# Kernel tuning notes

Hardware: AMD Instinct MI355X
Metric: run time of the kernel (lower is better)

## Reference

```python
import jax, jax.numpy as jnp
import numpy as np

B, N, D, H, L = 4, 1024, 256, 4, 2  # batch, nodes, mem_dim, heads, gcn sublayers
DK = D // H


def setup_inputs() -> dict:
    key = jax.random.key(0)
    ks = jax.random.split(key, 12)
    s = 0.05  # weight scale
    return {
        "gcn_inputs": jax.random.normal(ks[0], (B, N, D), jnp.float32),
        "rel_embs": jax.random.normal(ks[1], (B, N, D), jnp.float32),
        "adj": jax.random.randint(ks[2], (B, N, N), 0, 2, jnp.int32),
        "mask": jnp.zeros((B, 1, N), jnp.int32),  # 0 == valid token in this code's convention
        "W_Q": jax.random.normal(ks[3], (2 * D, D), jnp.float32) * s,
        "b_Q": jnp.zeros((D,), jnp.float32),
        "W_K": jax.random.normal(ks[4], (D, D), jnp.float32) * s,
        "b_K": jnp.zeros((D,), jnp.float32),
        "W_gcn": jax.random.normal(ks[5], (H * L, D, D), jnp.float32) * s,
        "b_gcn": jnp.zeros((H * L, D), jnp.float32),
        "W_out": jax.random.normal(ks[6], (D * H * L, D), jnp.float32) * s,
        "b_out": jnp.zeros((D,), jnp.float32),
    }


def _zscore_attn(scores, m, adj):
    """Faithful port of stdzscore + threshold + weightsoftmax chain.
    scores: [B,H,N,N]; m: bool [B,1,1,N] True=valid; adj: int [B,N,N]."""
    mf = m.astype(scores.dtype)
    # mymean (dim=[-1]): count from mask squeezed over dim -2 -> [B,1], +1e-4
    cnt_mean = mf[:, :, 0, :].sum(-1)[..., None] + 1e-4  # [B,1,1]
    ds = jnp.where(m, scores, 0.0).sum(-1)               # [B,H,N]
    mean = ds / cnt_mean                                  # [B,H,N]
    # mystd (dim=[-1]): count from full mask summed over -1 -> [B,1,1], +1e-4
    cnt_std = mf.sum(-1) + 1e-4                           # [B,1,1]
    sdata = jnp.where(m, (scores - mean[..., None]) ** 2, 0.0).sum(-1)
    std = jnp.sqrt(sdata / cnt_std + 1e-10)               # [B,H,N]
    z = (scores - mean[..., None]) / (std[..., None] + 1e-4)
    z = jnp.where(m, z, 0.0)
    thresh = z < 0
    s2 = jnp.where(thresh, -1e9, z)
    s2 = jnp.where(m, s2, -1e9)
    # weightsoftmax: stable exp, multiply by adjacency, mask, renormalize
    e = jnp.exp(s2 - s2.max(-1, keepdims=True))
    e = e * adj.astype(scores.dtype)[:, None]             # [B,H,N,N]
    e = jnp.where(m, e, 0.0) + 1e-10
    w = e / e.sum(-1, keepdims=True)
    w = jnp.where(m, w, 0.0)
    kill = (~m) | thresh | (adj == 0)[:, None]
    return jnp.where(kill, 0.0, w)


def reference(gcn_inputs, rel_embs, adj, mask, W_Q, b_Q, W_K, b_K, W_gcn, b_gcn, W_out, b_out):
    m = (mask == 0)[:, :, None, :]  # [B,1,1,N] True = valid
    # MultiHeadAttention: q from cat(query, rel), k from query
    q = (jnp.concatenate([gcn_inputs, rel_embs], -1) @ W_Q + b_Q)
    q = q.reshape(B, N, H, DK).transpose(0, 2, 1, 3)      # [B,H,N,DK]
    k = (gcn_inputs @ W_K + b_K).reshape(B, N, H, DK).transpose(0, 2, 1, 3)
    scores = jnp.einsum('bhnd,bhmd->bhnm', q, k)
    p_attn = _zscore_attn(scores, m, adj)                 # [B,H,N,N]
    # MultiGraphConvLayer (dropout = identity at inference)
    head_outs = []
    for i in range(H):
        a = p_attn[:, i]                                  # [B,N,N]
        denom = a.sum(2, keepdims=True) + 1.0             # [B,N,1]
        outputs = gcn_inputs
        layer_outs = []
        for l in range(L):
            idx = i * L + l
            Ax = jnp.einsum('bnm,bmd->bnd', a, outputs)
            # Linear applied to BOTH Ax and outputs (bias added twice, as in source)
            AxW = (Ax @ W_gcn[idx] + b_gcn[idx]) + (outputs @ W_gcn[idx] + b_gcn[idx])
            outputs = jax.nn.relu(AxW / denom)
            layer_outs.append(outputs)
        head_outs.append(jnp.concatenate(layer_outs, -1))  # [B,N,D*L]
    final = jnp.concatenate(head_outs, -1)                 # [B,N,D*L*H]
    return gcn_inputs + final @ W_out + b_out
```

## Files before the change

### kernel.cpp

```cpp
#include <hip/hip_runtime.h>
#include <math.h>

typedef unsigned short u16;
typedef __attribute__((ext_vector_type(8))) short short8;
typedef __attribute__((ext_vector_type(4))) float floatx4;

#define LDS_P 72

__device__ __forceinline__ float bf2f(u16 u) {
  union { unsigned int i; float f; } v; v.i = ((unsigned int)u) << 16; return v.f;
}
__device__ __forceinline__ u16 f2bf(float f) {
  union { float f; unsigned int i; } v; v.f = f;
  unsigned int x = v.i;
  return (u16)((x + 0x7FFFu + ((x >> 16) & 1u)) >> 16);
}

__device__ __forceinline__ void stage64(const u16* __restrict__ G, int ldg,
                                        u16* __restrict__ S, int tid) {
#pragma unroll
  for (int j = 0; j < 2; ++j) {
    int id = tid + (j << 8);
    int row = id >> 3, c8 = (id & 7) << 3;
    *reinterpret_cast<float4*>(S + row * LDS_P + c8) =
        *reinterpret_cast<const float4*>(G + (long long)row * ldg + c8);
  }
}

__device__ __forceinline__ void mfma_loop(const u16* __restrict__ A, int lda,
                                          const u16* __restrict__ Bt, int ldb,
                                          int K, u16* As, u16* Bs,
                                          floatx4 acc[2][2], int tid) {
  int lane = tid & 63;
  int wm = ((tid >> 6) & 1) << 5, wn = ((tid >> 6) >> 1) << 5;
  int lr = lane & 15, lq8 = (lane >> 4) << 3;
  for (int k0 = 0; k0 < K; k0 += 64) {
    stage64(A + k0, lda, As, tid);
    stage64(Bt + k0, ldb, Bs, tid);
    __syncthreads();
#pragma unroll
    for (int kc = 0; kc < 64; kc += 32) {
      short8 a0 = *reinterpret_cast<const short8*>(As + (wm + lr) * LDS_P + kc + lq8);
      short8 a1 = *reinterpret_cast<const short8*>(As + (wm + 16 + lr) * LDS_P + kc + lq8);
      short8 b0 = *reinterpret_cast<const short8*>(Bs + (wn + lr) * LDS_P + kc + lq8);
      short8 b1 = *reinterpret_cast<const short8*>(Bs + (wn + 16 + lr) * LDS_P + kc + lq8);
      acc[0][0] = __builtin_amdgcn_mfma_f32_16x16x32_bf16(a0, b0, acc[0][0], 0, 0, 0);
      acc[0][1] = __builtin_amdgcn_mfma_f32_16x16x32_bf16(a0, b1, acc[0][1], 0, 0, 0);
      acc[1][0] = __builtin_amdgcn_mfma_f32_16x16x32_bf16(a1, b0, acc[1][0], 0, 0, 0);
      acc[1][1] = __builtin_amdgcn_mfma_f32_16x16x32_bf16(a1, b1, acc[1][1], 0, 0, 0);
    }
    __syncthreads();
  }
}

#define EPI_SETUP                                                     \
  int lane = threadIdx.x & 63;                                        \
  int wm = ((threadIdx.x >> 6) & 1) << 5,                             \
      wn = ((threadIdx.x >> 6) >> 1) << 5;                            \
  int lr = lane & 15, lq4 = (lane >> 4) << 2;

__global__ __launch_bounds__(256) void proj2_k(
    const u16* __restrict__ A, const u16* __restrict__ WQT,
    const u16* __restrict__ WKT, const float* __restrict__ b_Q,
    const float* __restrict__ b_K, u16* __restrict__ qbf,
    u16* __restrict__ kbf) {
  __shared__ u16 As[64 * LDS_P], Bs[64 * LDS_P];
  int z = blockIdx.z;
  int m0 = blockIdx.y << 6, n0 = blockIdx.x << 6;
  int K = z ? 256 : 512, ldb = z ? 256 : 512;
  const u16* Bt = z ? WKT : WQT;
  const float* bias = z ? b_K : b_Q;
  u16* C = z ? kbf : qbf;
  floatx4 acc[2][2] = {};
  mfma_loop(A + (long long)m0 * 512, 512, Bt + (long long)n0 * ldb, ldb, K, As, Bs,
            acc, threadIdx.x);
  EPI_SETUP
#pragma unroll
  for (int ti = 0; ti < 2; ++ti)
#pragma unroll
    for (int tj = 0; tj < 2; ++tj)
#pragma unroll
      for (int r = 0; r < 4; ++r) {
        int row = m0 + wm + ti * 16 + lq4 + r;
        int col = n0 + wn + tj * 16 + lr;
        C[(long long)row * 256 + col] = f2bf(acc[ti][tj][r] + bias[col]);
      }
}

__global__ __launch_bounds__(256) void mscore_k(
    const u16* __restrict__ q, const u16* __restrict__ kb,
    u16* __restrict__ sc) {
  __shared__ u16 As[64 * LDS_P], Bs[64 * LDS_P];
  int z = blockIdx.z;
  int b = z & 3, h = z >> 2;
  int m0 = blockIdx.y << 6, n0 = blockIdx.x << 6;
  const u16* Ab = q + b * 262144 + h * 64;
  const u16* Bb = kb + b * 262144 + h * 64;
  floatx4 acc[2][2] = {};
  mfma_loop(Ab + (long long)m0 * 256, 256, Bb + (long long)n0 * 256, 256, 64, As, Bs,
            acc, threadIdx.x);
  u16* Cb = sc + ((long long)z << 20);
  EPI_SETUP
#pragma unroll
  for (int ti = 0; ti < 2; ++ti)
#pragma unroll
    for (int tj = 0; tj < 2; ++tj)
#pragma unroll
      for (int r = 0; r < 4; ++r) {
        int row = m0 + wm + ti * 16 + lq4 + r;
        int col = n0 + wn + tj * 16 + lr;
        Cb[(long long)row * 1024 + col] = f2bf(acc[ti][tj][r]);
      }
}

__device__ __forceinline__ float wred_sum(float v) {
#pragma unroll
  for (int m = 32; m > 0; m >>= 1) v += __shfl_xor(v, m, 64);
  return v;
}
__device__ __forceinline__ void wred_sum2(float& a, float& b) {
#pragma unroll
  for (int m = 32; m > 0; m >>= 1) {
    float ta = __shfl_xor(a, m, 64);
    float tb = __shfl_xor(b, m, 64);
    a += ta; b += tb;
  }
}
__device__ __forceinline__ float wred_max(float v) {
#pragma unroll
  for (int m = 32; m > 0; m >>= 1) v = fmaxf(v, __shfl_xor(v, m, 64));
  return v;
}

__global__ __launch_bounds__(256) void zscore_w(
    const u16* __restrict__ sc, const int* __restrict__ adj,
    const int* __restrict__ mask, u16* __restrict__ wout,
    float* __restrict__ denh) {
  int wv = threadIdx.x >> 6, lane = threadIdx.x & 63;
  int row = (blockIdx.x << 2) + wv;
  int b = row >> 10, n = row & 1023;
  int e0 = lane << 4;
  const int* arow = adj + ((long long)row << 10) + e0;
  const int* mrow = mask + (b << 10) + e0;

  unsigned int vbits = 0, abits = 0;
#pragma unroll
  for (int q = 0; q < 4; ++q) {
    int4 a4 = *reinterpret_cast<const int4*>(arow + (q << 2));
    int4 m4 = *reinterpret_cast<const int4*>(mrow + (q << 2));
    vbits |= (unsigned)(m4.x == 0) << (q * 4);
    vbits |= (unsigned)(m4.y == 0) << (q * 4 + 1);
    vbits |= (unsigned)(m4.z == 0) << (q * 4 + 2);
    vbits |= (unsigned)(m4.w == 0) << (q * 4 + 3);
    abits |= (unsigned)(a4.x != 0) << (q * 4);
    abits |= (unsigned)(a4.y != 0) << (q * 4 + 1);
    abits |= (unsigned)(a4.z != 0) << (q * 4 + 2);
    abits |= (unsigned)(a4.w != 0) << (q * 4 + 3);
  }
  float cnt = wred_sum((float)__popc(vbits));
  float cnteff = cnt + 0.0001f;

  for (int h = 0; h < 4; ++h) {
    int z = (h << 2) + b;
    const u16* srow = sc + ((long long)z << 20) + ((long long)n << 10) + e0;
    float s[16];
#pragma unroll
    for (int q = 0; q < 2; ++q) {
      uint4 u = *reinterpret_cast<const uint4*>(srow + (q << 3));
      unsigned int uu[4] = {u.x, u.y, u.z, u.w};
#pragma unroll
      for (int t = 0; t < 4; ++t) {
        union { unsigned int i; float f; } lo, hi;
        lo.i = uu[t] << 16;
        hi.i = uu[t] & 0xffff0000u;
        s[q * 8 + t * 2] = lo.f;
        s[q * 8 + t * 2 + 1] = hi.f;
      }
    }
    float suml = 0.f, sql = 0.f;
#pragma unroll
    for (int u = 0; u < 16; ++u)
      if ((vbits >> u) & 1) { suml += s[u]; sql += s[u] * s[u]; }
    wred_sum2(suml, sql);
    float mean = suml / cnteff;
    float sdata = sql - 2.f * mean * suml + cnt * mean * mean;
    float stdv = sqrtf(fmaxf(sdata, 0.f) / cnteff + 1e-10f);
    float inv = 1.f / (stdv + 0.0001f);

    float maxl = -1e9f;
#pragma unroll
    for (int u = 0; u < 16; ++u) {
      float zz = (s[u] - mean) * inv;
      int vv = (vbits >> u) & 1;
      zz = vv ? zz : 0.f;
      s[u] = zz;
      if (vv && zz >= 0.f) maxl = fmaxf(maxl, zz);
    }
    float rowmax = wred_max(maxl);

    float e[16], el = 0.f;
#pragma unroll
    for (int u = 0; u < 16; ++u) {
      int vv = (vbits >> u) & 1, aa = (abits >> u) & 1;
      float ev = (vv && aa && (s[u] >= 0.f)) ? expf(s[u] - rowmax) : 0.f;
      e[u] = ev + 1e-10f;
      el += e[u];
    }
    float esum = wred_sum(el);
    float rinv = 1.f / esum;

    float wl = 0.f;
    unsigned int wo[8];
#pragma unroll
    for (int u = 0; u < 16; u += 2) {
      int s0 = ((vbits >> u) & 1) && ((abits >> u) & 1) && (s[u] >= 0.f);
      int s1 = ((vbits >> (u + 1)) & 1) && ((abits >> (u + 1)) & 1) && (s[u + 1] >= 0.f);
      float w0 = s0 ? e[u] * rinv : 0.f;
      float w1 = s1 ? e[u + 1] * rinv : 0.f;
      wl += w0 + w1;
      wo[u >> 1] = (unsigned)f2bf(w0) | ((unsigned)f2bf(w1) << 16);
    }
    float wsum = wred_sum(wl);

    u16* orow = wout + ((size_t)z << 20) + ((size_t)n << 10) + e0;
    reinterpret_cast<uint4*>(orow)[0] = make_uint4(wo[0], wo[1], wo[2], wo[3]);
    reinterpret_cast<uint4*>(orow)[1] = make_uint4(wo[4], wo[5], wo[6], wo[7]);
    if (lane == 0) denh[(z << 10) + n] = wsum + 1.0f;
  }
}

__global__ __launch_bounds__(256) void gcn_k(
    const u16* __restrict__ wght, const u16* __restrict__ srcT,
    const u16* __restrict__ addsrc, int zmask, int ldadd, long long sAdd,
    const u16* __restrict__ WgT_all, const float* __restrict__ bg_all,
    const float* __restrict__ den, int l,
    u16* __restrict__ ob, u16* __restrict__ obT, u16* __restrict__ fin) {
  __shared__ u16 lds[35328];
  u16* As = lds;
  u16* Bs = lds + 4608;
  u16* Ts = lds;
  u16* Ws = lds + 16896;
  int tid = threadIdx.x;
  int m0 = blockIdx.x << 6;
  int z = blockIdx.y;
  int lane = tid & 63, w = tid >> 6;
  int lr = lane & 15, lq8 = (lane >> 4) << 3, lq4 = (lane >> 4) << 2;

  const u16* Aw = wght + ((long long)z << 20) + (long long)m0 * 1024;
  const u16* Bt = srcT + (long long)(z & zmask) * 262144;
  const u16* addb = addsrc + (long long)(z & zmask) * sAdd;
  int idx2 = (z >> 2) * 2 + l;
  const u16* Wg = WgT_all + (long long)idx2 * 65536;

  floatx4 acc[4][4] = {};
  for (int k0 = 0; k0 < 1024; k0 += 64) {
#pragma unroll
    for (int j = 0; j < 2; ++j) {
      int id = tid + (j << 8);
      int row = id >> 3, c8 = (id & 7) << 3;
      *reinterpret_cast<float4*>(As + row * 72 + c8) =
          *reinterpret_cast<const float4*>(Aw + (long long)row * 1024 + k0 + c8);
    }
#pragma unroll
    for (int j = 0; j < 8; ++j) {
      int id = tid + (j << 8);
      int row = id >> 3, c8 = (id & 7) << 3;
      *reinterpret_cast<float4*>(Bs + row * 72 + c8) =
          *reinterpret_cast<const float4*>(Bt + (long long)row * 1024 + k0 + c8);
    }
    __syncthreads();
#pragma unroll
    for (int kc = 0; kc < 64; kc += 32) {
      short8 a[4], b[4];
#pragma unroll
      for (int t = 0; t < 4; ++t) {
        a[t] = *reinterpret_cast<const short8*>(As + (t * 16 + lr) * 72 + kc + lq8);
        b[t] = *reinterpret_cast<const short8*>(Bs + ((w << 6) + t * 16 + lr) * 72 + kc + lq8);
      }
#pragma unroll
      for (int ti = 0; ti < 4; ++ti)
#pragma unroll
        for (int tj = 0; tj < 4; ++tj)
          acc[ti][tj] =
              __builtin_amdgcn_mfma_f32_16x16x32_bf16(a[ti], b[tj], acc[ti][tj], 0, 0, 0);
    }
    __syncthreads();
  }
#pragma unroll
  for (int ti = 0; ti < 4; ++ti)
#pragma unroll
    for (int tj = 0; tj < 4; ++tj)
#pragma unroll
      for (int r = 0; r < 4; ++r) {
        int row = ti * 16 + lq4 + r;
        int col = (w << 6) + tj * 16 + lr;
        float v = acc[ti][tj][r] + bf2f(addb[(long long)(m0 + row) * ldadd + col]);
        Ts[row * 264 + col] = f2bf(v);
        acc[ti][tj][r] = 0.f;
      }
  __syncthreads();
  for (int kc0 = 0; kc0 < 256; kc0 += 64) {
#pragma unroll
    for (int j = 0; j < 8; ++j) {
      int id = tid + (j << 8);
      int row = id >> 3, c8 = (id & 7) << 3;
      *reinterpret_cast<float4*>(Ws + row * 72 + c8) =
          *reinterpret_cast<const float4*>(Wg + (long long)row * 256 + kc0 + c8);
    }
    __syncthreads();
#pragma unroll
    for (int kc = 0; kc < 64; kc += 32) {
      short8 a[4], b[4];
#pragma unroll
      for (int t = 0; t < 4; ++t) {
        a[t] = *reinterpret_cast<const short8*>(Ts + (t * 16 + lr) * 264 + kc0 + kc + lq8);
        b[t] = *reinterpret_cast<const short8*>(Ws + ((w << 6) + t * 16 + lr) * 72 + kc + lq8);
      }
#pragma unroll
      for (int ti = 0; ti < 4; ++ti)
#pragma unroll
        for (int tj = 0; tj < 4; ++tj)
          acc[ti][tj] =
              __builtin_amdgcn_mfma_f32_16x16x32_bf16(a[ti], b[tj], acc[ti][tj], 0, 0, 0);
    }
    __syncthreads();
  }
  const float* bb = bg_all + idx2 * 256;
  const float* dn = den + (z << 10);
  long long finbase = (long long)(z & 3) * 2097152 + idx2 * 256;
#pragma unroll
  for (int ti = 0; ti < 4; ++ti) {
    int row = m0 + ti * 16 + lq4;
#pragma unroll
    for (int tj = 0; tj < 4; ++tj) {
      int col = (w << 6) + tj * 16 + lr;
      u16 bv4[4];
#pragma unroll
      for (int r = 0; r < 4; ++r) {
        float v = (acc[ti][tj][r] + 2.f * bb[col]) / dn[row + r];
        v = fmaxf(v, 0.f);
        bv4[r] = f2bf(v);
        fin[finbase + (long long)(row + r) * 2048 + col] = bv4[r];
        if (ob) ob[((long long)z << 18) + (long long)(row + r) * 256 + col] = bv4[r];
      }
      if (obT) {
        ushort4 t4 = {bv4[0], bv4[1], bv4[2], bv4[3]};
        *reinterpret_cast<ushort4*>(obT + ((long long)z << 18) +
                                    (long long)col * 1024 + row) = t4;
      }
    }
  }
}

__global__ __launch_bounds__(256) void mfinal_k(
    const u16* __restrict__ fin, const u16* __restrict__ WoT,
    float* __restrict__ out) {
  __shared__ u16 As[64 * LDS_P], Bs[64 * LDS_P];
  int m0 = blockIdx.y << 6, n0 = blockIdx.x << 6;
  int ks = blockIdx.z << 9;
  floatx4 acc[2][2] = {};
  mfma_loop(fin + (long long)m0 * 2048 + ks, 2048, WoT + (long long)n0 * 2048 + ks,
            2048, 512, As, Bs, acc, threadIdx.x);
  EPI_SETUP
#pragma unroll
  for (int ti = 0; ti < 2; ++ti)
#pragma unroll
    for (int tj = 0; tj < 2; ++tj)
#pragma unroll
      for (int r = 0; r < 4; ++r) {
        int row = m0 + wm + ti * 16 + lq4 + r;
        int col = n0 + wn + tj * 16 + lr;
        atomicAdd(out + (long long)row * 256 + col, acc[ti][tj][r]);
      }
}

__global__ __launch_bounds__(256) void prep_k(
    const float* __restrict__ X, const float* __restrict__ R,
    const float* __restrict__ W_Q, const float* __restrict__ W_K,
    const float* __restrict__ W_gcn, const float* __restrict__ W_out,
    const float* __restrict__ b_out,
    u16* __restrict__ A, u16* __restrict__ XT, u16* __restrict__ WQT,
    u16* __restrict__ WKT, u16* __restrict__ WgT, u16* __restrict__ WoT,
    float* __restrict__ out) {
  int gid = blockIdx.x * 256 + threadIdx.x;
  if (gid < 2097152) {
    int col = gid & 511, row = gid >> 9;
    float v = (col < 256) ? X[row * 256 + col] : R[row * 256 + col - 256];
    A[gid] = f2bf(v);
  } else if (gid < 3145728) {
    int t = gid - 2097152;
    int b = t >> 18, r2 = t & 262143;
    int i = r2 >> 8, j = r2 & 255;
    XT[b * 262144 + j * 1024 + i] = f2bf(X[t]);
  } else if (gid < 3276800) {
    int t = gid - 3145728;
    int i = t >> 8, j = t & 255;
    WQT[j * 512 + i] = f2bf(W_Q[t]);
  } else if (gid < 3342336) {
    int t = gid - 3276800;
    int i = t >> 8, j = t & 255;
    WKT[j * 256 + i] = f2bf(W_K[t]);
  } else if (gid < 3866624) {
    int t = gid - 3342336;
    int zz = t >> 16, r2 = t & 65535;
    int i = r2 >> 8, j = r2 & 255;
    WgT[zz * 65536 + j * 256 + i] = f2bf(W_gcn[t]);
  } else if (gid < 4390912) {
    int t = gid - 3866624;
    int i = t >> 8, j = t & 255;
    WoT[j * 2048 + i] = f2bf(W_out[t]);
  } else if (gid < 4653056) {
    int t = gid - 4390912;
    int col = (t << 2) & 255;
    float4 x = reinterpret_cast<const float4*>(X)[t];
    float4 b = *reinterpret_cast<const float4*>(b_out + col);
    x.x += b.x; x.y += b.y; x.z += b.z; x.w += b.w;
    reinterpret_cast<float4*>(out)[t] = x;
  }
}

extern "C" void kernel_launch(void* const* d_in, const int* in_sizes, int n_in,
                              void* d_out, int out_size, void* d_ws, size_t ws_size,
                              hipStream_t stream) {
  const float* X = (const float*)d_in[0];
  const float* R = (const float*)d_in[1];
  const int* adj = (const int*)d_in[2];
  const int* mask = (const int*)d_in[3];
  const float* W_Q = (const float*)d_in[4];
  const float* b_Q = (const float*)d_in[5];
  const float* W_K = (const float*)d_in[6];
  const float* b_K = (const float*)d_in[7];
  const float* W_gcn = (const float*)d_in[8];
  const float* b_gcn = (const float*)d_in[9];
  const float* W_out = (const float*)d_in[10];
  const float* b_out = (const float*)d_in[11];
  float* out = (float*)d_out;

  u16* wsu = (u16*)d_ws;
  u16* A_qk = wsu;
  u16* qbf  = A_qk + (2u << 20);
  u16* kbf  = qbf + (1u << 20);
  u16* XT   = kbf + (1u << 20);
  u16* WQT  = XT + (1u << 20);
  u16* WKT  = WQT + (1u << 17);
  u16* WgT  = WKT + (1u << 16);
  u16* WoT  = WgT + (1u << 19);
  u16* ob   = WoT + (1u << 19);
  u16* obT  = ob + (4u << 20);
  u16* finb = obT + (4u << 20);
  u16* wght = finb + (8u << 20);
  float* den = (float*)(wght + (16u << 20));
  u16* sc = (u16*)(den + (1 << 14));

  prep_k<<<18176, 256, 0, stream>>>(X, R, W_Q, W_K, W_gcn, W_out, b_out,
                                    A_qk, XT, WQT, WKT, WgT, WoT, out);

  proj2_k<<<dim3(4, 64, 2), 256, 0, stream>>>(A_qk, WQT, WKT, b_Q, b_K, qbf, kbf);

  mscore_k<<<dim3(16, 16, 16), 256, 0, stream>>>(qbf, kbf, sc);
  zscore_w<<<1024, 256, 0, stream>>>(sc, adj, mask, wght, den);

  gcn_k<<<dim3(16, 16), 256, 0, stream>>>(wght, XT, A_qk, 3, 512, 524288LL,
                                          WgT, b_gcn, den, 0, ob, obT, finb);
  gcn_k<<<dim3(16, 16), 256, 0, stream>>>(wght, obT, ob, 15, 256, 262144LL,
                                          WgT, b_gcn, den, 1, nullptr, nullptr, finb);

  mfinal_k<<<dim3(4, 64, 4), 256, 0, stream>>>(finb, WoT, out);
}
```

Baseline: 248.0 us.

## Register-prefetch GEMM tiles, halve gcn row tile, and tile-transpose weights in prep

The shared MFMA loop and gcn_k now load the next K-slice from global memory into registers while the current slice is computed from LDS, so memory latency overlaps compute. gcn_k moves from 64 to 32 rows per block, which doubles the grid to 512 blocks and cuts LDS use for better occupancy, but each block reloads the full B operand. prep_k now transposes the weights and XT through 64x64 LDS tiles, giving coalesced stores in place of strided scalar writes. Register pressure rises from the prefetch buffers (pb[8], pw[8]).

Result: slower. 356.0 us (+43.5%).

```diff
diff --git a/kernel.cpp b/kernel.cpp
--- a/kernel.cpp
+++ b/kernel.cpp
@@ -14,17 +14,6 @@
   union { float f; unsigned int i; } v; v.f = f;
   unsigned int x = v.i;
   return (u16)((x + 0x7FFFu + ((x >> 16) & 1u)) >> 16);
-}
-
-__device__ __forceinline__ void stage64(const u16* __restrict__ G, int ldg,
-                                        u16* __restrict__ S, int tid) {
-#pragma unroll
-  for (int j = 0; j < 2; ++j) {
-    int id = tid + (j << 8);
-    int row = id >> 3, c8 = (id & 7) << 3;
-    *reinterpret_cast<float4*>(S + row * LDS_P + c8) =
-        *reinterpret_cast<const float4*>(G + (long long)row * ldg + c8);
-  }
 }
 
 __device__ __forceinline__ void mfma_loop(const u16* __restrict__ A, int lda,
@@ -34,10 +23,29 @@
   int lane = tid & 63;
   int wm = ((tid >> 6) & 1) << 5, wn = ((tid >> 6) >> 1) << 5;
   int lr = lane & 15, lq8 = (lane >> 4) << 3;
+  int r0 = tid >> 3, c8 = (tid & 7) << 3;
+
+  const u16* pA0 = A + (long long)r0 * lda + c8;
+  const u16* pA1 = A + (long long)(r0 + 32) * lda + c8;
+  const u16* pB0 = Bt + (long long)r0 * ldb + c8;
+  const u16* pB1 = Bt + (long long)(r0 + 32) * ldb + c8;
+  float4 pa0 = *reinterpret_cast<const float4*>(pA0);
+  float4 pa1 = *reinterpret_cast<const float4*>(pA1);
+  float4 pb0 = *reinterpret_cast<const float4*>(pB0);
+  float4 pb1 = *reinterpret_cast<const float4*>(pB1);
+
   for (int k0 = 0; k0 < K; k0 += 64) {
-    stage64(A + k0, lda, As, tid);
-    stage64(Bt + k0, ldb, Bs, tid);
-    __syncthreads();
+    *reinterpret_cast<float4*>(As + r0 * LDS_P + c8) = pa0;
+    *reinterpret_cast<float4*>(As + (r0 + 32) * LDS_P + c8) = pa1;
+    *reinterpret_cast<float4*>(Bs + r0 * LDS_P + c8) = pb0;
+    *reinterpret_cast<float4*>(Bs + (r0 + 32) * LDS_P + c8) = pb1;
+    __syncthreads();
+    if (k0 + 64 < K) {
+      pa0 = *reinterpret_cast<const float4*>(pA0 + k0 + 64);
+      pa1 = *reinterpret_cast<const float4*>(pA1 + k0 + 64);
+      pb0 = *reinterpret_cast<const float4*>(pB0 + k0 + 64);
+      pb1 = *reinterpret_cast<const float4*>(pB1 + k0 + 64);
+    }
 #pragma unroll
     for (int kc = 0; kc < 64; kc += 32) {
       short8 a0 = *reinterpret_cast<const short8*>(As + (wm + lr) * LDS_P + kc + lq8);
@@ -235,13 +243,13 @@
     const u16* __restrict__ WgT_all, const float* __restrict__ bg_all,
     const float* __restrict__ den, int l,
     u16* __restrict__ ob, u16* __restrict__ obT, u16* __restrict__ fin) {
-  __shared__ u16 lds[35328];
+  __shared__ u16 lds[26880];
   u16* As = lds;
-  u16* Bs = lds + 4608;
+  u16* Bs = lds + 2304;
   u16* Ts = lds;
-  u16* Ws = lds + 16896;
+  u16* Ws = lds + 8448;
   int tid = threadIdx.x;
-  int m0 = blockIdx.x << 6;
+  int m0 = blockIdx.x << 5;
   int z = blockIdx.y;
   int lane = tid & 63, w = tid >> 6;
   int lr = lane & 15, lq8 = (lane >> 4) << 3, lq4 = (lane >> 4) << 2;
@@ -252,33 +260,47 @@
   int idx2 = (z >> 2) * 2 + l;
   const u16* Wg = WgT_all + (long long)idx2 * 65536;
 
-  floatx4 acc[4][4] = {};
+  int rA = tid >> 3, c8 = (tid & 7) << 3;
+  const u16* gA = Aw + (long long)rA * 1024 + c8;
+
+  floatx4 acc[2][4] = {};
+  float4 pa = *reinterpret_cast<const float4*>(gA);
+  float4 pb[8];
+#pragma unroll
+  for (int j = 0; j < 8; ++j) {
+    int id = tid + (j << 8);
+    pb[j] = *reinterpret_cast<const float4*>(Bt + (long long)(id >> 3) * 1024 +
+                                             ((id & 7) << 3));
+  }
+
   for (int k0 = 0; k0 < 1024; k0 += 64) {
-#pragma unroll
-    for (int j = 0; j < 2; ++j) {
-      int id = tid + (j << 8);
-      int row = id >> 3, c8 = (id & 7) << 3;
-      *reinterpret_cast<float4*>(As + row * 72 + c8) =
-          *reinterpret_cast<const float4*>(Aw + (long long)row * 1024 + k0 + c8);
-    }
+    *reinterpret_cast<float4*>(As + rA * 72 + c8) = pa;
 #pragma unroll
     for (int j = 0; j < 8; ++j) {
       int id = tid + (j << 8);
-      int row = id >> 3, c8 = (id & 7) << 3;
-      *reinterpret_cast<float4*>(Bs + row * 72 + c8) =
-          *reinterpret_cast<const float4*>(Bt + (long long)row * 1024 + k0 + c8);
-    }
-    __syncthreads();
+      *reinterpret_cast<float4*>(Bs + (id >> 3) * 72 + ((id & 7) << 3)) = pb[j];
+    }
+    __syncthreads();
+    if (k0 + 64 < 1024) {
+      pa = *reinterpret_cast<const float4*>(gA + k0 + 64);
+#pragma unroll
+      for (int j = 0; j < 8; ++j) {
+        int id = tid + (j << 8);
+        pb[j] = *reinterpret_cast<const float4*>(Bt + (long long)(id >> 3) * 1024 +
+                                                 k0 + 64 + ((id & 7) << 3));
+      }
+    }
 #pragma unroll
     for (int kc = 0; kc < 64; kc += 32) {
-      short8 a[4], b[4];
-#pragma unroll
-      for (int t = 0; t < 4; ++t) {
+      short8 a[2], b[4];
+#pragma unroll
+      for (int t = 0; t < 2; ++t)
         a[t] = *reinterpret_cast<const short8*>(As + (t * 16 + lr) * 72 + kc + lq8);
+#pragma unroll
+      for (int t = 0; t < 4; ++t)
         b[t] = *reinterpret_cast<const short8*>(Bs + ((w << 6) + t * 16 + lr) * 72 + kc + lq8);
-      }
-#pragma unroll
-      for (int ti = 0; ti < 4; ++ti)
+#pragma unroll
+      for (int ti = 0; ti < 2; ++ti)
 #pragma unroll
         for (int tj = 0; tj < 4; ++tj)
           acc[ti][tj] =
@@ -287,7 +309,7 @@
     __syncthreads();
   }
 #pragma unroll
-  for (int ti = 0; ti < 4; ++ti)
+  for (int ti = 0; ti < 2; ++ti)
 #pragma unroll
     for (int tj = 0; tj < 4; ++tj)
 #pragma unroll
@@ -298,26 +320,39 @@
         Ts[row * 264 + col] = f2bf(v);
         acc[ti][tj][r] = 0.f;
       }
-  __syncthreads();
+  float4 pw[8];
+#pragma unroll
+  for (int j = 0; j < 8; ++j) {
+    int id = tid + (j << 8);
+    pw[j] = *reinterpret_cast<const float4*>(Wg + (long long)(id >> 3) * 256 +
+                                             ((id & 7) << 3));
+  }
   for (int kc0 = 0; kc0 < 256; kc0 += 64) {
 #pragma unroll
     for (int j = 0; j < 8; ++j) {
       int id = tid + (j << 8);
-      int row = id >> 3, c8 = (id & 7) << 3;
-      *reinterpret_cast<float4*>(Ws + row * 72 + c8) =
-          *reinterpret_cast<const float4*>(Wg + (long long)row * 256 + kc0 + c8);
-    }
-    __syncthreads();
+      *reinterpret_cast<float4*>(Ws + (id >> 3) * 72 + ((id & 7) << 3)) = pw[j];
+    }
+    __syncthreads();
+    if (kc0 < 192) {
+#pragma unroll
+      for (int j = 0; j < 8; ++j) {
+        int id = tid + (j << 8);
+        pw[j] = *reinterpret_cast<const float4*>(Wg + (long long)(id >> 3) * 256 +
+                                                 kc0 + 64 + ((id & 7) << 3));
+      }
+    }
 #pragma unroll
     for (int kc = 0; kc < 64; kc += 32) {
-      short8 a[4], b[4];
-#pragma unroll
-      for (int t = 0; t < 4; ++t) {
+      short8 a[2], b[4];
+#pragma unroll
+      for (int t = 0; t < 2; ++t)
         a[t] = *reinterpret_cast<const short8*>(Ts + (t * 16 + lr) * 264 + kc0 + kc + lq8);
+#pragma unroll
+      for (int t = 0; t < 4; ++t)
         b[t] = *reinterpret_cast<const short8*>(Ws + ((w << 6) + t * 16 + lr) * 72 + kc + lq8);
-      }
-#pragma unroll
-      for (int ti = 0; ti < 4; ++ti)
+#pragma unroll
+      for (int ti = 0; ti < 2; ++ti)
 #pragma unroll
         for (int tj = 0; tj < 4; ++tj)
           acc[ti][tj] =
@@ -329,7 +364,7 @@
   const float* dn = den + (z << 10);
   long long finbase = (long long)(z & 3) * 2097152 + idx2 * 256;
 #pragma unroll
-  for (int ti = 0; ti < 4; ++ti) {
+  for (int ti = 0; ti < 2; ++ti) {
     int row = m0 + ti * 16 + lq4;
 #pragma unroll
     for (int tj = 0; tj < 4; ++tj) {
@@ -382,35 +417,55 @@
     u16* __restrict__ A, u16* __restrict__ XT, u16* __restrict__ WQT,
     u16* __restrict__ WKT, u16* __restrict__ WgT, u16* __restrict__ WoT,
     float* __restrict__ out) {
-  int gid = blockIdx.x * 256 + threadIdx.x;
-  if (gid < 2097152) {
+  int bi = blockIdx.x;
+  int tid = threadIdx.x;
+  if (bi < 560) {
+    __shared__ u16 tile[64 * LDS_P];
+    const float* S;
+    u16* D;
+    int I, ti, tj;
+    if (bi < 256) {
+      int zz = bi >> 6, rem = bi & 63;
+      ti = rem >> 2; tj = rem & 3; I = 1024;
+      S = X + zz * 262144; D = XT + zz * 262144;
+    } else if (bi < 288) {
+      int t = bi - 256; ti = t >> 2; tj = t & 3; I = 512;
+      S = W_Q; D = WQT;
+    } else if (bi < 304) {
+      int t = bi - 288; ti = t >> 2; tj = t & 3; I = 256;
+      S = W_K; D = WKT;
+    } else if (bi < 432) {
+      int t = bi - 304; int zz = t >> 4, rem = t & 15;
+      ti = rem >> 2; tj = rem & 3; I = 256;
+      S = W_gcn + zz * 65536; D = WgT + zz * 65536;
+    } else {
+      int t = bi - 432; ti = t >> 2; tj = t & 3; I = 2048;
+      S = W_out; D = WoT;
+    }
+    int rr = tid >> 4, cc = (tid & 15) << 2;
+#pragma unroll
+    for (int q = 0; q < 4; ++q) {
+      int r = rr + (q << 4);
+      float4 v = *reinterpret_cast<const float4*>(S + (long long)(ti * 64 + r) * 256 +
+                                                  tj * 64 + cc);
+      ushort4 h = {f2bf(v.x), f2bf(v.y), f2bf(v.z), f2bf(v.w)};
+      *reinterpret_cast<ushort4*>(tile + r * LDS_P + cc) = h;
+    }
+    __syncthreads();
+    int jl = tid >> 2, il = (tid & 3) << 4;
+    u16 vals[16];
+#pragma unroll
+    for (int u = 0; u < 16; ++u) vals[u] = tile[(il + u) * LDS_P + jl];
+    u16* dp = D + (long long)(tj * 64 + jl) * I + ti * 64 + il;
+    reinterpret_cast<uint4*>(dp)[0] = *reinterpret_cast<uint4*>(vals);
+    reinterpret_cast<uint4*>(dp)[1] = *reinterpret_cast<uint4*>(vals + 8);
+  } else if (bi < 8752) {
+    int gid = (bi - 560) * 256 + tid;
     int col = gid & 511, row = gid >> 9;
     float v = (col < 256) ? X[row * 256 + col] : R[row * 256 + col - 256];
     A[gid] = f2bf(v);
-  } else if (gid < 3145728) {
-    int t = gid - 2097152;
-    int b = t >> 18, r2 = t & 262143;
-    int i = r2 >> 8, j = r2 & 255;
-    XT[b * 262144 + j * 1024 + i] = f2bf(X[t]);
-  } else if (gid < 3276800) {
-    int t = gid - 3145728;
-    int i = t >> 8, j = t & 255;
-    WQT[j * 512 + i] = f2bf(W_Q[t]);
-  } else if (gid < 3342336) {
-    int t = gid - 3276800;
-    int i = t >> 8, j = t & 255;
-    WKT[j * 256 + i] = f2bf(W_K[t]);
-  } else if (gid < 3866624) {
-    int t = gid - 3342336;
-    int zz = t >> 16, r2 = t & 65535;
-    int i = r2 >> 8, j = r2 & 255;
-    WgT[zz * 65536 + j * 256 + i] = f2bf(W_gcn[t]);
-  } else if (gid < 4390912) {
-    int t = gid - 3866624;
-    int i = t >> 8, j = t & 255;
-    WoT[j * 2048 + i] = f2bf(W_out[t]);
-  } else if (gid < 4653056) {
-    int t = gid - 4390912;
+  } else {
+    int t = (bi - 8752) * 256 + tid;
     int col = (t << 2) & 255;
     float4 x = reinterpret_cast<const float4*>(X)[t];
     float4 b = *reinterpret_cast<const float4*>(b_out + col);
@@ -452,17 +507,17 @@
   float* den = (float*)(wght + (16u << 20));
   u16* sc = (u16*)(den + (1 << 14));
 
-  prep_k<<<18176, 256, 0, stream>>>(X, R, W_Q, W_K, W_gcn, W_out, b_out,
-                                    A_qk, XT, WQT, WKT, WgT, WoT, out);
+  prep_k<<<9776, 256, 0, stream>>>(X, R, W_Q, W_K, W_gcn, W_out, b_out,
+                                   A_qk, XT, WQT, WKT, WgT, WoT, out);
 
   proj2_k<<<dim3(4, 64, 2), 256, 0, stream>>>(A_qk, WQT, WKT, b_Q, b_K, qbf, kbf);
 
   mscore_k<<<dim3(16, 16, 16), 256, 0, stream>>>(qbf, kbf, sc);
   zscore_w<<<1024, 256, 0, stream>>>(sc, adj, mask, wght, den);
 
-  gcn_k<<<dim3(16, 16), 256, 0, stream>>>(wght, XT, A_qk, 3, 512, 524288LL,
+  gcn_k<<<dim3(32, 16), 256, 0, stream>>>(wght, XT, A_qk, 3, 512, 524288LL,
                                           WgT, b_gcn, den, 0, ob, obT, finb);
-  gcn_k<<<dim3(16, 16), 256, 0, stream>>>(wght, obT, ob, 15, 256, 262144LL,
+  gcn_k<<<dim3(32, 16), 256, 0, stream>>>(wght, obT, ob, 15, 256, 262144LL,
                                           WgT, b_gcn, den, 1, nullptr, nullptr, finb);
 
   mfinal_k<<<dim3(4, 64, 4), 256, 0, stream>>>(finb, WoT, out);
```
